# Kernel optimization log

Measured on AMD Instinct MI355X. Metric: run time of the kernel, lower is better.

Reference implementation:

```python
import jax, jax.numpy as jnp
import numpy as np

EPS = 1e-6
NUM_HEADS = 16

def layernorm(x, alpha, bias):
    # Faithful to the torch module: torch.std uses ddof=1, and eps is added to std.
    mean = jnp.mean(x, axis=-1, keepdims=True)
    std = jnp.std(x, axis=-1, keepdims=True, ddof=1)
    return alpha * (x - mean) / (std + EPS) + bias

def setup_inputs() -> dict:
    key = jax.random.key(0)
    B, S, D, F = 4, 2048, 1024, 4096
    ks = jax.random.split(key, 8)
    s = 1.0 / np.sqrt(D)
    inp = {
        'x': jax.random.normal(ks[0], (B, S, D), jnp.float32),
        'src_mask': jnp.ones((B, 1, 1, S), jnp.int32),
        'wq': jax.random.normal(ks[1], (D, D), jnp.float32) * s,
        'bq': jnp.zeros((D,), jnp.float32),
        'wk': jax.random.normal(ks[2], (D, D), jnp.float32) * s,
        'bk': jnp.zeros((D,), jnp.float32),
        'wv': jax.random.normal(ks[3], (D, D), jnp.float32) * s,
        'bv': jnp.zeros((D,), jnp.float32),
        'wo': jax.random.normal(ks[4], (D, D), jnp.float32) * s,
        'bo': jnp.zeros((D,), jnp.float32),
        'w1': jax.random.normal(ks[5], (D, F), jnp.float32) * s,
        'b1': jnp.zeros((F,), jnp.float32),
        'w2': jax.random.normal(ks[6], (F, D), jnp.float32) * (1.0 / np.sqrt(F)),
        'b2': jnp.zeros((D,), jnp.float32),
        'ln1_a': jnp.ones((D,), jnp.float32),
        'ln1_b': jnp.zeros((D,), jnp.float32),
        'ln2_a': jnp.ones((D,), jnp.float32),
        'ln2_b': jnp.zeros((D,), jnp.float32),
    }
    return inp

def mha(x, src_mask, wq, bq, wk, bk, wv, bv, wo, bo):
    B, S, D = x.shape
    H = NUM_HEADS
    dk = D // H
    q = (x @ wq + bq).reshape(B, S, H, dk).transpose(0, 2, 1, 3)  # [B,H,S,dk]
    k = (x @ wk + bk).reshape(B, S, H, dk).transpose(0, 2, 1, 3)
    v = (x @ wv + bv).reshape(B, S, H, dk).transpose(0, 2, 1, 3)
    scores = jnp.einsum('bhqd,bhkd->bhqk', q, k) / np.sqrt(dk)  # [B,H,S,S]
    scores = jnp.where(src_mask == 0, -1e9, scores)
    p = jax.nn.softmax(scores, axis=-1)
    ctx = jnp.einsum('bhqk,bhkd->bhqd', p, v)  # [B,H,S,dk]
    ctx = ctx.transpose(0, 2, 1, 3).reshape(B, S, D)
    return ctx @ wo + bo

def reference(x, src_mask, wq, bq, wk, bk, wv, bv, wo, bo,
              w1, b1, w2, b2, ln1_a, ln1_b, ln2_a, ln2_b):
    # residual 1: pre-norm self-attention (dropout is identity in eval)
    h = x + mha(layernorm(x, ln1_a, ln1_b), src_mask, wq, bq, wk, bk, wv, bv, wo, bo)
    # residual 2: pre-norm FFN
    hn = layernorm(h, ln2_a, ln2_b)
    ffn = jax.nn.relu(hn @ w1 + b1) @ w2 + b2
    return h + ffn
```

## Files before the change

### kernel.cpp

```cpp
#include <hip/hip_runtime.h>
#include <hip/hip_bf16.h>

typedef __attribute__((ext_vector_type(8))) short bf16x8;
typedef __attribute__((ext_vector_type(4))) short bf16x4;
typedef __attribute__((ext_vector_type(4))) float f32x4;
typedef __hip_bfloat16 bf16;
typedef unsigned short u16;

#define B_ 4
#define S_ 2048
#define D_ 1024
#define F_ 4096
#define H_ 16
#define MROWS 8192
#define QSCALE 0.18033688011116012f

__device__ __forceinline__ unsigned pkbf(float lo, float hi){
  union{float f; unsigned u;} a, b; a.f = lo; b.f = hi;
  return __builtin_amdgcn_perm(b.u + 0x8000u, a.u + 0x8000u, 0x07060302);
}
__device__ __forceinline__ u16 f2bf_bits(float f){
  union{bf16 h; u16 u;} x; x.h = __float2bfloat16(f); return x.u;
}
__device__ __forceinline__ void gll16(const bf16* gp, u16* lp){
  __builtin_amdgcn_global_load_lds(
      (const __attribute__((address_space(1))) void*)gp,
      (__attribute__((address_space(3))) void*)lp, 16, 0, 0);
}

struct Ptr4 { const float* p[4]; };
__global__ __launch_bounds__(256) void transpose4_to_bf16(
    Ptr4 ws_, bf16* __restrict__ WT)
{
  __shared__ float t[32][33];
  const float* W = ws_.p[blockIdx.z];
  bf16* dst = WT + (size_t)blockIdx.z*1024*1024;
  int n0 = blockIdx.x*32, k0 = blockIdx.y*32;
  int x = threadIdx.x, y = threadIdx.y;
  #pragma unroll
  for (int i=0;i<32;i+=8)
    t[y+i][x] = W[(size_t)(k0+y+i)*1024 + n0+x];
  __syncthreads();
  #pragma unroll
  for (int i=0;i<32;i+=8)
    dst[(size_t)(n0+y+i)*1024 + k0+x] = __float2bfloat16(t[x][y+i]);
}

__global__ __launch_bounds__(256) void transpose_to_bf16(
    const float* __restrict__ W, bf16* __restrict__ WT, int K, int N)
{
  __shared__ float t[32][33];
  int n0 = blockIdx.x*32, k0 = blockIdx.y*32;
  int x = threadIdx.x, y = threadIdx.y;
  #pragma unroll
  for (int i=0;i<32;i+=8)
    t[y+i][x] = W[(size_t)(k0+y+i)*N + n0+x];
  __syncthreads();
  #pragma unroll
  for (int i=0;i<32;i+=8)
    WT[(size_t)(n0+y+i)*K + k0+x] = __float2bfloat16(t[x][y+i]);
}

__global__ __launch_bounds__(256) void concat_bias(
    const float* __restrict__ bq, const float* __restrict__ bk,
    const float* __restrict__ bv, float* __restrict__ out)
{
  int i = blockIdx.x*256 + threadIdx.x;
  float v = (i < 1024) ? bq[i] : (i < 2048) ? bk[i-1024] : bv[i-2048];
  out[i] = v;
}

__global__ __launch_bounds__(256) void v_transpose(
    const bf16* __restrict__ qkv, bf16* __restrict__ vT)
{
  __shared__ u16 tile[64*65];
  const int bh = blockIdx.y, b = bh>>4, h = bh&15;
  const int s0 = blockIdx.x*64;
  const int tid = threadIdx.x;
  const bf16* src = qkv + (size_t)(b*S_ + s0)*3072 + 2048 + h*64;
  #pragma unroll
  for (int i=0;i<2;i++){
    int idx = i*256 + tid;
    int r = idx>>3, sg = idx&7;
    uint4 v = *reinterpret_cast<const uint4*>(src + (size_t)r*3072 + sg*8);
    const u16* e = (const u16*)&v;
    #pragma unroll
    for (int j=0;j<8;j++) tile[r*65 + sg*8 + j] = e[j];
  }
  __syncthreads();
  bf16* dst = vT + (size_t)bh*64*S_ + s0;
  #pragma unroll
  for (int i=0;i<2;i++){
    int idx = i*256 + tid;
    int d = idx>>3, sg = idx&7;
    u16 tmp[8];
    #pragma unroll
    for (int j=0;j<8;j++) tmp[j] = tile[(sg*8+j)*65 + d];
    *reinterpret_cast<uint4*>(dst + (size_t)d*S_ + sg*8) = *reinterpret_cast<uint4*>(tmp);
  }
}

__device__ __forceinline__ float block_reduce_256(float v, float* sbuf){
  #pragma unroll
  for (int o=32;o>0;o>>=1) v += __shfl_down(v, o);
  int wave = threadIdx.x>>6;
  if ((threadIdx.x&63)==0) sbuf[wave] = v;
  __syncthreads();
  float r = sbuf[0]+sbuf[1]+sbuf[2]+sbuf[3];
  __syncthreads();
  return r;
}

__global__ __launch_bounds__(256) void ln_fwd(
    const float* __restrict__ x, const float* __restrict__ alpha,
    const float* __restrict__ beta, bf16* __restrict__ out)
{
  __shared__ float sbuf[4];
  int row = blockIdx.x, tid = threadIdx.x;
  const float4* xr = reinterpret_cast<const float4*>(x + (size_t)row*D_);
  float4 v = xr[tid];
  float sum = block_reduce_256(v.x+v.y+v.z+v.w, sbuf);
  float mean = sum * (1.0f/1024.0f);
  float dx0=v.x-mean, dx1=v.y-mean, dx2=v.z-mean, dx3=v.w-mean;
  float ssq = block_reduce_256(dx0*dx0+dx1*dx1+dx2*dx2+dx3*dx3, sbuf);
  float std_ = sqrtf(ssq * (1.0f/1023.0f));
  float inv = 1.0f/(std_ + 1e-6f);
  const float4* ar = reinterpret_cast<const float4*>(alpha);
  const float4* br = reinterpret_cast<const float4*>(beta);
  float4 a = ar[tid], bb = br[tid];
  unsigned* o = reinterpret_cast<unsigned*>(out + (size_t)row*D_);
  o[tid*2+0] = pkbf(a.x*dx0*inv + bb.x, a.y*dx1*inv + bb.y);
  o[tid*2+1] = pkbf(a.z*dx2*inv + bb.z, a.w*dx3*inv + bb.w);
}

template<int EPI, int TN>
__global__ __launch_bounds__(256) void gemm_bt(
    const bf16* __restrict__ A, const bf16* __restrict__ BT,
    const float* __restrict__ bias, const float* __restrict__ res,
    void* __restrict__ out, int M, int N, int K)
{
  __shared__ __align__(16) u16 As[128*32];
  __shared__ __align__(16) u16 Bs[TN*32];
  const int tid = threadIdx.x;
  const int m0 = blockIdx.x*128, n0 = blockIdx.y*TN;
  const int wave = tid>>6, lane = tid&63;
  const int wm = (wave>>1)*64, wn = (wave&1)*(TN/2);
  const int lrow = lane&15, quad = lane>>4;
  constexpr int BNT = TN/32;
  const int srow = wave*32 + (lane>>2);
  const int sseg = lane&3;
  const bf16* apg = A + (size_t)(m0+srow)*K + sseg*8;
  u16* asd = &As[wave*1024];
  const int brow = wave*(TN/4) + (lane>>2);
  const bf16* bpg = BT + (size_t)(n0+brow)*K + sseg*8;
  u16* bsd = &Bs[wave*(TN*8)];

  f32x4 acc[4][BNT];
  #pragma unroll
  for (int i=0;i<4;i++)
    #pragma unroll
    for (int j=0;j<BNT;j++) acc[i][j] = (f32x4){0.f,0.f,0.f,0.f};

  for (int k0=0; k0<K; k0+=32) {
    gll16(apg + k0,                 asd);
    gll16(apg + k0 + (size_t)16*K,  asd + 512);
    gll16(bpg + k0,                 bsd);
    if (TN == 128) gll16(bpg + k0 + (size_t)16*K, bsd + 512);
    __syncthreads();
    bf16x8 a[4], b[BNT];
    #pragma unroll
    for (int t=0;t<4;t++)
      a[t] = *reinterpret_cast<const bf16x8*>(&As[(wm + t*16 + lrow)*32 + quad*8]);
    #pragma unroll
    for (int t=0;t<BNT;t++)
      b[t] = *reinterpret_cast<const bf16x8*>(&Bs[(wn + t*16 + lrow)*32 + quad*8]);
    #pragma unroll
    for (int mt=0;mt<4;mt++)
      #pragma unroll
      for (int nt=0;nt<BNT;nt++)
        acc[mt][nt] = __builtin_amdgcn_mfma_f32_16x16x32_bf16(a[mt], b[nt], acc[mt][nt], 0,0,0);
    __syncthreads();
  }

  #pragma unroll
  for (int mt=0;mt<4;mt++){
    #pragma unroll
    for (int nt=0;nt<BNT;nt++){
      int col = n0 + wn + nt*16 + lrow;
      float bv = bias[col];
      float sc = (EPI == 3 && col < 1024) ? QSCALE : 1.0f;
      #pragma unroll
      for (int r=0;r<4;r++){
        int row = m0 + wm + mt*16 + quad*4 + r;
        size_t idx = (size_t)row*N + col;
        float val = acc[mt][nt][r] + bv;
        if (EPI == 1) val = fmaxf(val, 0.0f);
        if (EPI == 3) val *= sc;
        if (EPI == 2) {
          ((float*)out)[idx] = val + res[idx];
        } else {
          ((bf16*)out)[idx] = __float2bfloat16(val);
        }
      }
    }
  }
}

#define KP 72

__global__ __launch_bounds__(512) void flash_attn_mfma(
    const bf16* __restrict__ qkv, const bf16* __restrict__ vT,
    const int* __restrict__ mask, bf16* __restrict__ ctx)
{
  __shared__ __align__(16) u16 Ks[64*KP];
  __shared__ __align__(16) u16 Vt[64*KP];
  __shared__ __align__(16) float Mb[64];

  const int b = blockIdx.z, h = blockIdx.y, qt = blockIdx.x;
  const int tid = threadIdx.x, wave = tid>>6, lane = tid&63;
  const int lr = lane&15, quad = lane>>4;
  const int qbase = qt*256 + wave*32;

  const bf16* base = qkv + (size_t)b*S_*3072 + h*64;
  const bf16* vtb  = vT + (size_t)(b*H_+h)*64*S_;
  const int*  mrow = mask + b*S_;

  bf16x8 qf[2][2];
  #pragma unroll
  for (int c=0;c<2;c++){
    const bf16* qp = base + (size_t)(qbase + c*16 + lr)*3072 + quad*8;
    qf[c][0] = *reinterpret_cast<const bf16x8*>(qp);
    qf[c][1] = *reinterpret_cast<const bf16x8*>(qp + 32);
  }

  const bf16x4 ones4 = {(short)0x3F80,(short)0x3F80,(short)0x3F80,(short)0x3F80};

  f32x4 actx[2][4];
  f32x4 acc_l[2];
  #pragma unroll
  for (int c=0;c<2;c++){
    #pragma unroll
    for (int dt=0;dt<4;dt++) actx[c][dt] = (f32x4){0.f,0.f,0.f,0.f};
    acc_l[c] = (f32x4){0.f,0.f,0.f,0.f};
  }

  const int sr = tid>>3, sg = tid&7;

  for (int kt=0; kt<S_; kt+=64){
    *reinterpret_cast<uint4*>(&Ks[sr*KP + sg*8]) =
      *reinterpret_cast<const uint4*>(base + 1024 + (size_t)(kt+sr)*3072 + sg*8);
    *reinterpret_cast<uint4*>(&Vt[sr*KP + sg*8]) =
      *reinterpret_cast<const uint4*>(vtb + (size_t)sr*S_ + kt + sg*8);
    if (tid < 64) Mb[tid] = (mrow[kt+tid]==0) ? -2e9f : 0.0f;
    unsigned long long bal = __ballot(mrow[kt + lane] == 0);
    __syncthreads();

    bf16x4 pk[2][4];
    if (bal == 0ULL) {
      #pragma unroll
      for (int nt=0;nt<4;nt++){
        bf16x8 kf0 = *reinterpret_cast<const bf16x8*>(&Ks[(nt*16+lr)*KP + quad*8]);
        bf16x8 kf1 = *reinterpret_cast<const bf16x8*>(&Ks[(nt*16+lr)*KP + 32 + quad*8]);
        #pragma unroll
        for (int c=0;c<2;c++){
          f32x4 a = (f32x4){0.f,0.f,0.f,0.f};
          a = __builtin_amdgcn_mfma_f32_16x16x32_bf16(kf0, qf[c][0], a, 0,0,0);
          a = __builtin_amdgcn_mfma_f32_16x16x32_bf16(kf1, qf[c][1], a, 0,0,0);
          uint2 w;
          w.x = pkbf(__builtin_amdgcn_exp2f(a[0]), __builtin_amdgcn_exp2f(a[1]));
          w.y = pkbf(__builtin_amdgcn_exp2f(a[2]), __builtin_amdgcn_exp2f(a[3]));
          union{uint2 u; bf16x4 v;} cvt; cvt.u = w;
          pk[c][nt] = cvt.v;
        }
      }
    } else {
      #pragma unroll
      for (int nt=0;nt<4;nt++){
        bf16x8 kf0 = *reinterpret_cast<const bf16x8*>(&Ks[(nt*16+lr)*KP + quad*8]);
        bf16x8 kf1 = *reinterpret_cast<const bf16x8*>(&Ks[(nt*16+lr)*KP + 32 + quad*8]);
        float4 mb = *reinterpret_cast<const float4*>(&Mb[nt*16 + quad*4]);
        #pragma unroll
        for (int c=0;c<2;c++){
          f32x4 a = (f32x4){0.f,0.f,0.f,0.f};
          a = __builtin_amdgcn_mfma_f32_16x16x32_bf16(kf0, qf[c][0], a, 0,0,0);
          a = __builtin_amdgcn_mfma_f32_16x16x32_bf16(kf1, qf[c][1], a, 0,0,0);
          uint2 w;
          w.x = pkbf(__builtin_amdgcn_exp2f(a[0]+mb.x), __builtin_amdgcn_exp2f(a[1]+mb.y));
          w.y = pkbf(__builtin_amdgcn_exp2f(a[2]+mb.z), __builtin_amdgcn_exp2f(a[3]+mb.w));
          union{uint2 u; bf16x4 v;} cvt; cvt.u = w;
          pk[c][nt] = cvt.v;
        }
      }
    }

    #pragma unroll
    for (int dt=0;dt<4;dt++){
      #pragma unroll
      for (int kc=0;kc<4;kc++){
        bf16x4 vf = *reinterpret_cast<const bf16x4*>(&Vt[(dt*16+lr)*KP + kc*16 + quad*4]);
        #pragma unroll
        for (int c=0;c<2;c++)
          actx[c][dt] = __builtin_amdgcn_mfma_f32_16x16x16bf16_1k(vf, pk[c][kc], actx[c][dt], 0,0,0);
      }
    }
    #pragma unroll
    for (int kc=0;kc<4;kc++)
      #pragma unroll
      for (int c=0;c<2;c++)
        acc_l[c] = __builtin_amdgcn_mfma_f32_16x16x16bf16_1k(ones4, pk[c][kc], acc_l[c], 0,0,0);
    __syncthreads();
  }

  #pragma unroll
  for (int c=0;c<2;c++){
    float inv = 1.0f/acc_l[c][0];
    int q = qbase + c*16 + lr;
    bf16* op = ctx + (size_t)(b*S_+q)*D_ + h*64 + quad*4;
    #pragma unroll
    for (int dt=0;dt<4;dt++){
      uint2 o;
      o.x = pkbf(actx[c][dt][0]*inv, actx[c][dt][1]*inv);
      o.y = pkbf(actx[c][dt][2]*inv, actx[c][dt][3]*inv);
      *reinterpret_cast<uint2*>(op + dt*16) = o;
    }
  }
}

extern "C" void kernel_launch(void* const* d_in, const int* in_sizes, int n_in,
                              void* d_out, int out_size, void* d_ws, size_t ws_size,
                              hipStream_t stream) {
  const float* x    = (const float*)d_in[0];
  const int*   mask = (const int*)  d_in[1];
  const float* wq   = (const float*)d_in[2];
  const float* bq   = (const float*)d_in[3];
  const float* wk   = (const float*)d_in[4];
  const float* bk   = (const float*)d_in[5];
  const float* wv   = (const float*)d_in[6];
  const float* bv   = (const float*)d_in[7];
  const float* wo   = (const float*)d_in[8];
  const float* bo   = (const float*)d_in[9];
  const float* w1   = (const float*)d_in[10];
  const float* b1   = (const float*)d_in[11];
  const float* w2   = (const float*)d_in[12];
  const float* b2   = (const float*)d_in[13];
  const float* ln1a = (const float*)d_in[14];
  const float* ln1b = (const float*)d_in[15];
  const float* ln2a = (const float*)d_in[16];
  const float* ln2b = (const float*)d_in[17];

  char* ws = (char*)d_ws;
  bf16*  wqkvT = (bf16*) (ws + 0);
  bf16*  woT   = (bf16*) (ws + 6291456);
  bf16*  w1T   = (bf16*) (ws + 8388608);
  bf16*  w2T   = (bf16*) (ws + 16777216);
  float* bqkv  = (float*)(ws + 25165824);
  bf16*  xn    = (bf16*) (ws + 25178112);
  bf16*  vT    = (bf16*) (ws + 25178112);
  bf16*  qkv   = (bf16*) (ws + 41955328);
  bf16*  ctx   = (bf16*) (ws + 92286976);
  bf16*  hn    = (bf16*) (ws + 109064192);
  bf16*  act   = (bf16*) (ws + 25178112);

  dim3 tb(32,8);
  Ptr4 wp; wp.p[0]=wq; wp.p[1]=wk; wp.p[2]=wv; wp.p[3]=wo;
  transpose4_to_bf16<<<dim3(32,32,4),tb,0,stream>>>(wp, wqkvT);
  transpose_to_bf16<<<dim3(128,32),tb,0,stream>>>(w1, w1T, 1024,4096);
  transpose_to_bf16<<<dim3(32,128),tb,0,stream>>>(w2, w2T, 4096,1024);
  concat_bias<<<12,256,0,stream>>>(bq,bk,bv,bqkv);

  ln_fwd<<<8192,256,0,stream>>>(x, ln1a, ln1b, xn);
  gemm_bt<3,128><<<dim3(64,24),256,0,stream>>>(xn, wqkvT, bqkv, nullptr, qkv, MROWS,3072,1024);
  v_transpose<<<dim3(32,64),256,0,stream>>>(qkv, vT);
  flash_attn_mfma<<<dim3(S_/256,H_,B_),512,0,stream>>>(qkv, vT, mask, ctx);
  gemm_bt<2,64><<<dim3(64,16),256,0,stream>>>(ctx, woT, bo, x, d_out, MROWS,1024,1024);
  ln_fwd<<<8192,256,0,stream>>>((const float*)d_out, ln2a, ln2b, hn);
  gemm_bt<1,128><<<dim3(64,32),256,0,stream>>>(hn, w1T, b1, nullptr, act, MROWS,F_,1024);
  gemm_bt<2,64><<<dim3(64,16),256,0,stream>>>(act, w2T, b2, (const float*)d_out, d_out, MROWS,1024,F_);
}
```

Measured before the change: 563.8 us.

## Merge weight prep kernels and switch GEMM to 512-thread 128x128 tiles

Folds the three weight-transpose kernels and the bias concat into one prep launch to cut launch overhead. The GEMM moves to 8 waves per block on a fixed 128x128 tile, so each wave holds a 64x32 sub-tile. The Wo and W2 GEMMs now use 128-wide N tiles, which halves their grid. The bf16 epilogue store uses a manual rounding helper instead of __float2bfloat16. The larger tiles change occupancy and wave count, and the smaller grid for the N=1024 GEMMs may leave CUs underfilled.

```diff
diff --git a/kernel.cpp b/kernel.cpp
--- a/kernel.cpp
+++ b/kernel.cpp
@@ -19,8 +19,9 @@
   union{float f; unsigned u;} a, b; a.f = lo; b.f = hi;
   return __builtin_amdgcn_perm(b.u + 0x8000u, a.u + 0x8000u, 0x07060302);
 }
-__device__ __forceinline__ u16 f2bf_bits(float f){
-  union{bf16 h; u16 u;} x; x.h = __float2bfloat16(f); return x.u;
+__device__ __forceinline__ u16 bfrnd(float f){
+  union{float ff; unsigned u;} c; c.ff = f;
+  return (u16)((c.u + 0x8000u) >> 16);
 }
 __device__ __forceinline__ void gll16(const bf16* gp, u16* lp){
   __builtin_amdgcn_global_load_lds(
@@ -28,46 +29,30 @@
       (__attribute__((address_space(3))) void*)lp, 16, 0, 0);
 }
 
-struct Ptr4 { const float* p[4]; };
-__global__ __launch_bounds__(256) void transpose4_to_bf16(
-    Ptr4 ws_, bf16* __restrict__ WT)
-{
-  __shared__ float t[32][33];
-  const float* W = ws_.p[blockIdx.z];
-  bf16* dst = WT + (size_t)blockIdx.z*1024*1024;
-  int n0 = blockIdx.x*32, k0 = blockIdx.y*32;
-  int x = threadIdx.x, y = threadIdx.y;
-  #pragma unroll
-  for (int i=0;i<32;i+=8)
-    t[y+i][x] = W[(size_t)(k0+y+i)*1024 + n0+x];
-  __syncthreads();
-  #pragma unroll
-  for (int i=0;i<32;i+=8)
-    dst[(size_t)(n0+y+i)*1024 + k0+x] = __float2bfloat16(t[x][y+i]);
-}
-
-__global__ __launch_bounds__(256) void transpose_to_bf16(
-    const float* __restrict__ W, bf16* __restrict__ WT, int K, int N)
-{
-  __shared__ float t[32][33];
-  int n0 = blockIdx.x*32, k0 = blockIdx.y*32;
-  int x = threadIdx.x, y = threadIdx.y;
-  #pragma unroll
-  for (int i=0;i<32;i+=8)
-    t[y+i][x] = W[(size_t)(k0+y+i)*N + n0+x];
-  __syncthreads();
-  #pragma unroll
-  for (int i=0;i<32;i+=8)
-    WT[(size_t)(n0+y+i)*K + k0+x] = __float2bfloat16(t[x][y+i]);
-}
-
-__global__ __launch_bounds__(256) void concat_bias(
-    const float* __restrict__ bq, const float* __restrict__ bk,
-    const float* __restrict__ bv, float* __restrict__ out)
-{
-  int i = blockIdx.x*256 + threadIdx.x;
-  float v = (i < 1024) ? bq[i] : (i < 2048) ? bk[i-1024] : bv[i-2048];
-  out[i] = v;
+struct PrepArgs { const float* w[6]; const float* b[3]; };
+__global__ __launch_bounds__(256) void prep(
+    PrepArgs pa, bf16* __restrict__ wqkvoT, bf16* __restrict__ w1T,
+    bf16* __restrict__ w2T, float* __restrict__ bqkv)
+{
+  __shared__ float tl[32][33];
+  const int bid = blockIdx.x, tid = threadIdx.x;
+  const int x = tid&31, y = tid>>5;
+  if (bid < 12288) {
+    const float* W; bf16* dst; int K, N, nb, kb;
+    if (bid < 4096)      { int wi=bid>>10, t=bid&1023; W=pa.w[wi]; dst=wqkvoT+(size_t)wi*1048576; K=1024; N=1024; nb=t&31;  kb=t>>5; }
+    else if (bid < 8192) { int t=bid-4096;             W=pa.w[4];  dst=w1T;  K=1024; N=4096; nb=t&127; kb=t>>7; }
+    else                 { int t=bid-8192;             W=pa.w[5];  dst=w2T;  K=4096; N=1024; nb=t&31;  kb=t>>5; }
+    const int n0=nb*32, k0=kb*32;
+    #pragma unroll
+    for (int i=0;i<32;i+=8)
+      tl[y+i][x] = W[(size_t)(k0+y+i)*N + n0+x];
+    __syncthreads();
+    #pragma unroll
+    for (int i=0;i<32;i+=8)
+      dst[(size_t)(n0+y+i)*K + k0+x] = __float2bfloat16(tl[x][y+i]);
+  } else {
+    for (int i=tid; i<3072; i+=256) bqkv[i] = pa.b[i>>10][i&1023];
+  }
 }
 
 __global__ __launch_bounds__(256) void v_transpose(
@@ -133,51 +118,47 @@
   o[tid*2+1] = pkbf(a.z*dx2*inv + bb.z, a.w*dx3*inv + bb.w);
 }
 
-template<int EPI, int TN>
-__global__ __launch_bounds__(256) void gemm_bt(
+template<int EPI>
+__global__ __launch_bounds__(512) void gemm_bt(
     const bf16* __restrict__ A, const bf16* __restrict__ BT,
     const float* __restrict__ bias, const float* __restrict__ res,
     void* __restrict__ out, int M, int N, int K)
 {
   __shared__ __align__(16) u16 As[128*32];
-  __shared__ __align__(16) u16 Bs[TN*32];
+  __shared__ __align__(16) u16 Bs[128*32];
   const int tid = threadIdx.x;
-  const int m0 = blockIdx.x*128, n0 = blockIdx.y*TN;
+  const int m0 = blockIdx.x*128, n0 = blockIdx.y*128;
   const int wave = tid>>6, lane = tid&63;
-  const int wm = (wave>>1)*64, wn = (wave&1)*(TN/2);
+  const int wm = (wave>>2)*64, wn = (wave&3)*32;
   const int lrow = lane&15, quad = lane>>4;
-  constexpr int BNT = TN/32;
-  const int srow = wave*32 + (lane>>2);
+  const int srow = wave*16 + (lane>>2);
   const int sseg = lane&3;
-  const bf16* apg = A + (size_t)(m0+srow)*K + sseg*8;
-  u16* asd = &As[wave*1024];
-  const int brow = wave*(TN/4) + (lane>>2);
-  const bf16* bpg = BT + (size_t)(n0+brow)*K + sseg*8;
-  u16* bsd = &Bs[wave*(TN*8)];
-
-  f32x4 acc[4][BNT];
+  const bf16* apg = A  + (size_t)(m0+srow)*K + sseg*8;
+  const bf16* bpg = BT + (size_t)(n0+srow)*K + sseg*8;
+  u16* asd = &As[wave*512];
+  u16* bsd = &Bs[wave*512];
+
+  f32x4 acc[4][2];
   #pragma unroll
   for (int i=0;i<4;i++)
     #pragma unroll
-    for (int j=0;j<BNT;j++) acc[i][j] = (f32x4){0.f,0.f,0.f,0.f};
+    for (int j=0;j<2;j++) acc[i][j] = (f32x4){0.f,0.f,0.f,0.f};
 
   for (int k0=0; k0<K; k0+=32) {
-    gll16(apg + k0,                 asd);
-    gll16(apg + k0 + (size_t)16*K,  asd + 512);
-    gll16(bpg + k0,                 bsd);
-    if (TN == 128) gll16(bpg + k0 + (size_t)16*K, bsd + 512);
-    __syncthreads();
-    bf16x8 a[4], b[BNT];
+    gll16(apg + k0, asd);
+    gll16(bpg + k0, bsd);
+    __syncthreads();
+    bf16x8 a[4], b[2];
     #pragma unroll
     for (int t=0;t<4;t++)
       a[t] = *reinterpret_cast<const bf16x8*>(&As[(wm + t*16 + lrow)*32 + quad*8]);
     #pragma unroll
-    for (int t=0;t<BNT;t++)
+    for (int t=0;t<2;t++)
       b[t] = *reinterpret_cast<const bf16x8*>(&Bs[(wn + t*16 + lrow)*32 + quad*8]);
     #pragma unroll
     for (int mt=0;mt<4;mt++)
       #pragma unroll
-      for (int nt=0;nt<BNT;nt++)
+      for (int nt=0;nt<2;nt++)
         acc[mt][nt] = __builtin_amdgcn_mfma_f32_16x16x32_bf16(a[mt], b[nt], acc[mt][nt], 0,0,0);
     __syncthreads();
   }
@@ -185,7 +166,7 @@
   #pragma unroll
   for (int mt=0;mt<4;mt++){
     #pragma unroll
-    for (int nt=0;nt<BNT;nt++){
+    for (int nt=0;nt<2;nt++){
       int col = n0 + wn + nt*16 + lrow;
       float bv = bias[col];
       float sc = (EPI == 3 && col < 1024) ? QSCALE : 1.0f;
@@ -199,7 +180,7 @@
         if (EPI == 2) {
           ((float*)out)[idx] = val + res[idx];
         } else {
-          ((bf16*)out)[idx] = __float2bfloat16(val);
+          ((u16*)out)[idx] = bfrnd(val);
         }
       }
     }
@@ -361,19 +342,17 @@
   bf16*  hn    = (bf16*) (ws + 109064192);
   bf16*  act   = (bf16*) (ws + 25178112);
 
-  dim3 tb(32,8);
-  Ptr4 wp; wp.p[0]=wq; wp.p[1]=wk; wp.p[2]=wv; wp.p[3]=wo;
-  transpose4_to_bf16<<<dim3(32,32,4),tb,0,stream>>>(wp, wqkvT);
-  transpose_to_bf16<<<dim3(128,32),tb,0,stream>>>(w1, w1T, 1024,4096);
-  transpose_to_bf16<<<dim3(32,128),tb,0,stream>>>(w2, w2T, 4096,1024);
-  concat_bias<<<12,256,0,stream>>>(bq,bk,bv,bqkv);
+  PrepArgs pa;
+  pa.w[0]=wq; pa.w[1]=wk; pa.w[2]=wv; pa.w[3]=wo; pa.w[4]=w1; pa.w[5]=w2;
+  pa.b[0]=bq; pa.b[1]=bk; pa.b[2]=bv;
+  prep<<<12289,256,0,stream>>>(pa, wqkvT, w1T, w2T, bqkv);
 
   ln_fwd<<<8192,256,0,stream>>>(x, ln1a, ln1b, xn);
-  gemm_bt<3,128><<<dim3(64,24),256,0,stream>>>(xn, wqkvT, bqkv, nullptr, qkv, MROWS,3072,1024);
+  gemm_bt<3><<<dim3(64,24),512,0,stream>>>(xn, wqkvT, bqkv, nullptr, qkv, MROWS,3072,1024);
   v_transpose<<<dim3(32,64),256,0,stream>>>(qkv, vT);
   flash_attn_mfma<<<dim3(S_/256,H_,B_),512,0,stream>>>(qkv, vT, mask, ctx);
-  gemm_bt<2,64><<<dim3(64,16),256,0,stream>>>(ctx, woT, bo, x, d_out, MROWS,1024,1024);
+  gemm_bt<2><<<dim3(64,8),512,0,stream>>>(ctx, woT, bo, x, d_out, MROWS,1024,1024);
   ln_fwd<<<8192,256,0,stream>>>((const float*)d_out, ln2a, ln2b, hn);
-  gemm_bt<1,128><<<dim3(64,32),256,0,stream>>>(hn, w1T, b1, nullptr, act, MROWS,F_,1024);
-  gemm_bt<2,64><<<dim3(64,16),256,0,stream>>>(act, w2T, b2, (const float*)d_out, d_out, MROWS,1024,F_);
-}
+  gemm_bt<1><<<dim3(64,32),512,0,stream>>>(hn, w1T, b1, nullptr, act, MROWS,F_,1024);
+  gemm_bt<2><<<dim3(64,8),512,0,stream>>>(act, w2T, b2, (const float*)d_out, d_out, MROWS,1024,F_);
+}
```

After: 555.5 us. About the same (-1.5%).
